# Performance work log

Measured on AMD Instinct MI355X. Metric: run time of the kernel, lower is better.

## Reference

```python
import jax, jax.numpy as jnp
import numpy as np

NUM_HEADS = 8
NUM_GROUPS = 32
EPS = 1e-5

def group_norm(x, w, b):
    B, C, H, W = x.shape
    xg = x.reshape(B, NUM_GROUPS, -1)
    mean = xg.mean(axis=-1, keepdims=True)
    var = xg.var(axis=-1, keepdims=True)
    xg = (xg - mean) * jax.lax.rsqrt(var + EPS)
    return xg.reshape(B, C, H, W) * w[None, :, None, None] + b[None, :, None, None]

def setup_inputs() -> dict:
    key = jax.random.key(0)
    ks = jax.random.split(key, 3)
    B, C, H, W = 16, 512, 32, 32
    x = jax.random.normal(ks[0], (B, C, H, W), dtype=jnp.float32)
    norm_w = jnp.ones((C,), jnp.float32)
    norm_b = jnp.zeros((C,), jnp.float32)
    qkv_w = jax.random.normal(ks[1], (3 * C, C), dtype=jnp.float32) * (C ** -0.5)
    qkv_b = jnp.zeros((3 * C,), jnp.float32)
    proj_w = jax.random.normal(ks[2], (C, C), dtype=jnp.float32) * (C ** -0.5)
    proj_b = jnp.zeros((C,), jnp.float32)
    return {"x": x, "norm_w": norm_w, "norm_b": norm_b, "qkv_w": qkv_w,
            "qkv_b": qkv_b, "proj_w": proj_w, "proj_b": proj_b}

def reference(x, norm_w, norm_b, qkv_w, qkv_b, proj_w, proj_b):
    B, C, H, W = x.shape
    nh, hd = NUM_HEADS, C // NUM_HEADS
    L = H * W
    h = group_norm(x, norm_w, norm_b)
    # 1x1 conv == channel matmul
    qkv = jnp.einsum('oc,bcl->bol', qkv_w, h.reshape(B, C, L)) + qkv_b[None, :, None]
    qkv = qkv.reshape(B, 3, nh, hd, L)
    qkv = jnp.transpose(qkv, (1, 0, 2, 4, 3))  # (3, B, nh, L, hd)
    q, k, v = qkv[0], qkv[1], qkv[2]
    scale = hd ** -0.5
    attn = jax.nn.softmax(jnp.einsum('bnqd,bnkd->bnqk', q, k) * scale, axis=-1)
    h = jnp.einsum('bnqk,bnkd->bnqd', attn, v)          # (B, nh, L, hd)
    h = jnp.transpose(h, (0, 1, 3, 2)).reshape(B, C, L)  # (B, C, L)
    h = jnp.einsum('oc,bcl->bol', proj_w, h) + proj_b[None, :, None]
    return h.reshape(B, C, H, W) + x
```

## Files before the change

kernel.cpp:

```cpp
#include <hip/hip_runtime.h>
#include <hip/hip_bf16.h>

#define BATCH 16
#define CCH   512
#define LSEQ  1024
#define NH    8
#define HD    64
#define NG    32
#define CPG   16
#define EPS   1e-5f

typedef __attribute__((ext_vector_type(8))) short short8;
typedef __attribute__((ext_vector_type(4))) float f32x4;
#define MFMA __builtin_amdgcn_mfma_f32_16x16x32_bf16

__device__ inline short f2bf(float f) {
  unsigned u = __float_as_uint(f);
  u += 0x7FFFu + ((u >> 16) & 1u);
  return (short)(u >> 16);
}

__device__ inline void gl2lds16(const short* g, short* l) {
  __builtin_amdgcn_global_load_lds(
      (const __attribute__((address_space(1))) unsigned*)g,
      (__attribute__((address_space(3))) unsigned*)l, 16, 0, 0);
}
#define VMCNT0() asm volatile("s_waitcnt vmcnt(0)" ::: "memory")

__global__ __launch_bounds__(256) void cvt_kernel(const float* __restrict__ src,
                                                  short* __restrict__ dst) {
  const int i = blockIdx.x * 256 + threadIdx.x;
  const float4 v = ((const float4*)src)[i];
  short vals[4] = {f2bf(v.x), f2bf(v.y), f2bf(v.z), f2bf(v.w)};
  *(uint2*)(dst + (size_t)i * 4) = *(uint2*)vals;
}

__global__ __launch_bounds__(256) void gn_kernel(
    const float* __restrict__ x, const float* __restrict__ nw,
    const float* __restrict__ nb, short* __restrict__ hT)
{
  const int g = blockIdx.x, b = blockIdx.y;
  const size_t base = ((size_t)b * CCH + (size_t)g * CPG) * LSEQ;
  const float4* __restrict__ x4 = (const float4*)(x + base);
  const int tid = threadIdx.x;

  __shared__ short T[16][1026];
  __shared__ float red0[4], red1[4];

  float4 v[16];
  float s = 0.f, s2 = 0.f;
#pragma unroll
  for (int r = 0; r < 16; ++r) {
    v[r] = x4[tid + 256 * r];
    s  += (v[r].x + v[r].y) + (v[r].z + v[r].w);
    s2 += (v[r].x * v[r].x + v[r].y * v[r].y) + (v[r].z * v[r].z + v[r].w * v[r].w);
  }
#pragma unroll
  for (int m = 1; m < 64; m <<= 1) { s += __shfl_xor(s, m); s2 += __shfl_xor(s2, m); }
  const int wid = tid >> 6;
  if ((tid & 63) == 0) { red0[wid] = s; red1[wid] = s2; }
  __syncthreads();
  const float ts  = (red0[0] + red0[1]) + (red0[2] + red0[3]);
  const float ts2 = (red1[0] + red1[1]) + (red1[2] + red1[3]);
  const float mean = ts * (1.f / 16384.f);
  const float var  = ts2 * (1.f / 16384.f) - mean * mean;
  const float rstd = rsqrtf(var + EPS);
#pragma unroll
  for (int r = 0; r < 16; ++r) {
    const int e = tid + 256 * r;
    const int c = e >> 8, l4 = (e & 255) * 4;
    const float sc = rstd * nw[g * CPG + c];
    const float sh = nb[g * CPG + c] - mean * sc;
    T[c][l4 + 0] = f2bf(v[r].x * sc + sh);
    T[c][l4 + 1] = f2bf(v[r].y * sc + sh);
    T[c][l4 + 2] = f2bf(v[r].z * sc + sh);
    T[c][l4 + 3] = f2bf(v[r].w * sc + sh);
  }
  __syncthreads();
  short* __restrict__ outp = hT + (size_t)b * LSEQ * CCH + g * CPG;
#pragma unroll
  for (int it = 0; it < 4; ++it) {
    const int l = tid + 256 * it;
    short vals[16];
#pragma unroll
    for (int c = 0; c < 16; ++c) vals[c] = T[c][l];
    *(short8*)(outp + (size_t)l * CCH)     = *(short8*)&vals[0];
    *(short8*)(outp + (size_t)l * CCH + 8) = *(short8*)&vals[8];
  }
}

__global__ __launch_bounds__(256) void qkv_gemm(
    const short* __restrict__ Wb, const float* __restrict__ bias,
    const short* __restrict__ hT, short* __restrict__ qT,
    short* __restrict__ kT, short* __restrict__ vv)
{
  const int b = blockIdx.z, my = blockIdx.y;
  const int m0 = my * 128, n0 = blockIdx.x * 128;
  const short* __restrict__ Bsrc = hT + (size_t)b * LSEQ * CCH;

  __shared__ short smem[32768];
  const int tid = threadIdx.x, lane = tid & 63, w = tid >> 6;
  const int wm = (w >> 1) * 64, wn = (w & 1) * 64;
  const int l15 = lane & 15, l4g = lane >> 4;
  const int sr = lane >> 3, c8 = ((lane & 7) ^ (lane >> 3)) * 8;
  const int swz = (l15 & 7) << 4;

  const f32x4 fz = {0.f, 0.f, 0.f, 0.f};
  f32x4 acc[4][4];
#pragma unroll
  for (int i = 0; i < 4; ++i)
#pragma unroll
    for (int j = 0; j < 4; ++j) acc[i][j] = fz;

#define QSTAGE(ks, bb)                                                        \
  {                                                                           \
    const int k0_ = (ks) * 64;                                                \
    _Pragma("unroll")                                                         \
    for (int i_ = 0; i_ < 4; ++i_) {                                          \
      const int rb_ = w * 32 + i_ * 8;                                        \
      gl2lds16(Wb   + (size_t)(m0 + rb_ + sr) * CCH + k0_ + c8,               \
               &smem[(bb) * 8192 + rb_ * 64]);                                \
      gl2lds16(Bsrc + (size_t)(n0 + rb_ + sr) * CCH + k0_ + c8,               \
               &smem[16384 + (bb) * 8192 + rb_ * 64]);                        \
    }                                                                         \
  }

  QSTAGE(0, 0);
  VMCNT0();
  __syncthreads();

  for (int ks = 0; ks < 8; ++ks) {
    const int bb = ks & 1;
    if (ks < 7) QSTAGE(ks + 1, bb ^ 1);
#pragma unroll
    for (int kk = 0; kk < 2; ++kk) {
      const int ko = (kk * 64 + l4g * 16) ^ swz;
      short8 af[4], bf[4];
#pragma unroll
      for (int i = 0; i < 4; ++i)
        af[i] = *(const short8*)((const char*)&smem[bb * 8192 + (wm + i * 16 + l15) * 64] + ko);
#pragma unroll
      for (int j = 0; j < 4; ++j)
        bf[j] = *(const short8*)((const char*)&smem[16384 + bb * 8192 + (wn + j * 16 + l15) * 64] + ko);
#pragma unroll
      for (int i = 0; i < 4; ++i)
#pragma unroll
        for (int j = 0; j < 4; ++j)
          acc[i][j] = MFMA(af[i], bf[j], acc[i][j], 0, 0, 0);
    }
    VMCNT0();
    __syncthreads();
  }

  const int region = my >> 2;
  const float scale = (region == 0) ? 0.125f : 1.0f;
  short (*CT)[136] = (short (*)[136])smem;

#pragma unroll
  for (int i = 0; i < 4; ++i)
#pragma unroll
    for (int r = 0; r < 4; ++r) {
      const int cl = wm + i * 16 + l4g * 4 + r;
      const float bb = bias[m0 + cl];
#pragma unroll
      for (int j = 0; j < 4; ++j) {
        const int ll = wn + j * 16 + l15;
        const short bv = f2bf((acc[i][j][r] + bb) * scale);
        if (region == 2) CT[cl][ll] = bv; else CT[ll][cl] = bv;
      }
    }
  __syncthreads();
#pragma unroll
  for (int it = 0; it < 8; ++it) {
    const int f = tid + it * 256;
    const int rr = f >> 4, cc8 = (f & 15) * 8;
    const short8 val = *(const short8*)&CT[rr][cc8];
    if (region == 2) {
      *(short8*)(vv + (size_t)b * CCH * LSEQ + (size_t)((my & 3) * 128 + rr) * LSEQ + n0 + cc8) = val;
    } else {
      short* __restrict__ dst = (region == 0) ? qT : kT;
      *(short8*)(dst + (size_t)b * LSEQ * CCH + (size_t)(n0 + rr) * CCH + (my & 3) * 128 + cc8) = val;
    }
  }
}

__global__ __launch_bounds__(256) void attn_kernel(
    const short* __restrict__ qT, const short* __restrict__ kT,
    const short* __restrict__ vv, short* __restrict__ oT)
{
  const int qt = blockIdx.x, hh = blockIdx.y, b = blockIdx.z;
  const int l0 = qt * 64, h64 = hh * 64;
  const int tid = threadIdx.x, lane = tid & 63, w = tid >> 6;
  const int l15 = lane & 15, l4g = lane >> 4;
  const int wq = w * 16;

  __shared__ short Ks[2][64][64];
  __shared__ short Vs[2][64][64];
  __shared__ unsigned Pw[4][16][36];

  const short* __restrict__ qb = qT + (size_t)b * LSEQ * CCH;
  const short* __restrict__ kb = kT + (size_t)b * LSEQ * CCH;
  const short* __restrict__ vb = vv + (size_t)b * CCH * LSEQ;

  short8 qf[2];
#pragma unroll
  for (int kk = 0; kk < 2; ++kk)
    qf[kk] = *(const short8*)(qb + (size_t)(l0 + wq + l15) * CCH + h64 + kk * 32 + l4g * 8);

  const f32x4 fz = {0.f, 0.f, 0.f, 0.f};
  f32x4 o[4];
#pragma unroll
  for (int df = 0; df < 4; ++df) o[df] = fz;
  float mr = -1.0e30f, lr = 0.f;

  const int sr = lane >> 3, c8 = ((lane & 7) ^ (lane >> 3)) * 8;
  const int swz = (l15 & 7) << 4;

#define ASTAGE(jt_, bb)                                                       \
  {                                                                           \
    const int j0_ = (jt_) * 64;                                               \
    _Pragma("unroll")                                                         \
    for (int i_ = 0; i_ < 2; ++i_) {                                          \
      const int rb_ = w * 16 + i_ * 8;                                        \
      gl2lds16(kb + (size_t)(j0_ + rb_ + sr) * CCH + h64 + c8,                \
               &Ks[bb][rb_][0]);                                              \
      gl2lds16(vb + (size_t)(h64 + rb_ + sr) * LSEQ + j0_ + c8,               \
               &Vs[bb][rb_][0]);                                              \
    }                                                                         \
  }

  ASTAGE(0, 0);
  VMCNT0();
  __syncthreads();

  for (int jt = 0; jt < 16; ++jt) {
    const int bb = jt & 1;
    if (jt < 15) ASTAGE(jt + 1, bb ^ 1);

    f32x4 s[4];
#pragma unroll
    for (int j = 0; j < 4; ++j) s[j] = fz;
#pragma unroll
    for (int kk = 0; kk < 2; ++kk) {
      const int ko = (kk * 64 + l4g * 16) ^ swz;
      short8 kf[4];
#pragma unroll
      for (int j = 0; j < 4; ++j)
        kf[j] = *(const short8*)((const char*)&Ks[bb][j * 16 + l15][0] + ko);
#pragma unroll
      for (int j = 0; j < 4; ++j) s[j] = MFMA(kf[j], qf[kk], s[j], 0, 0, 0);
    }

    float mx = s[0][0];
#pragma unroll
    for (int j = 0; j < 4; ++j)
#pragma unroll
      for (int r = 0; r < 4; ++r) mx = fmaxf(mx, s[j][r]);
    mx = fmaxf(mx, __shfl_xor(mx, 16));
    mx = fmaxf(mx, __shfl_xor(mx, 32));
    const float mnew = fmaxf(mr, mx);
    const float corr = __expf(mr - mnew);
    mr = mnew;

    float rs = 0.f;
    unsigned pk[4][2];
#pragma unroll
    for (int j = 0; j < 4; ++j) {
      float p0 = __expf(s[j][0] - mnew), p1 = __expf(s[j][1] - mnew);
      float p2 = __expf(s[j][2] - mnew), p3 = __expf(s[j][3] - mnew);
      rs += (p0 + p1) + (p2 + p3);
      __hip_bfloat162 w0 = __float22bfloat162_rn(make_float2(p0, p1));
      __hip_bfloat162 w1 = __float22bfloat162_rn(make_float2(p2, p3));
      pk[j][0] = *(unsigned*)&w0;
      pk[j][1] = *(unsigned*)&w1;
    }
    rs += __shfl_xor(rs, 16);
    rs += __shfl_xor(rs, 32);
    lr = lr * corr + rs;

#pragma unroll
    for (int j = 0; j < 4; ++j)
      *(uint2*)&Pw[w][l15][j * 8 + l4g * 2] = make_uint2(pk[j][0], pk[j][1]);

    float cb[4];
#pragma unroll
    for (int r = 0; r < 4; ++r) cb[r] = __shfl(corr, l4g * 4 + r);
#pragma unroll
    for (int df = 0; df < 4; ++df)
#pragma unroll
      for (int r = 0; r < 4; ++r) o[df][r] *= cb[r];

#pragma unroll
    for (int kk = 0; kk < 2; ++kk) {
      const short8 pf = *(const short8*)&Pw[w][l15][kk * 16 + l4g * 4];
      const int ko = (kk * 64 + l4g * 16) ^ swz;
#pragma unroll
      for (int df = 0; df < 4; ++df) {
        const short8 vf = *(const short8*)((const char*)&Vs[bb][df * 16 + l15][0] + ko);
        o[df] = MFMA(pf, vf, o[df], 0, 0, 0);
      }
    }
    VMCNT0();
    __syncthreads();
  }

  float lb[4];
#pragma unroll
  for (int r = 0; r < 4; ++r) lb[r] = 1.f / __shfl(lr, l4g * 4 + r);
  short* __restrict__ ob = oT + (size_t)b * LSEQ * CCH;
#pragma unroll
  for (int df = 0; df < 4; ++df)
#pragma unroll
    for (int r = 0; r < 4; ++r)
      ob[(size_t)(l0 + wq + l4g * 4 + r) * CCH + h64 + df * 16 + l15] = f2bf(o[df][r] * lb[r]);
}

__global__ __launch_bounds__(256) void proj_gemm(
    const short* __restrict__ Wb, const float* __restrict__ bias,
    const short* __restrict__ oT, const float* __restrict__ x,
    float* __restrict__ out)
{
  const int b = blockIdx.z;
  const int m0 = blockIdx.y * 128, n0 = blockIdx.x * 128;
  const short* __restrict__ Bsrc = oT + (size_t)b * LSEQ * CCH;

  __shared__ short smem[32768];
  const int tid = threadIdx.x, lane = tid & 63, w = tid >> 6;
  const int wm = (w >> 1) * 64, wn = (w & 1) * 64;
  const int l15 = lane & 15, l4g = lane >> 4;
  const int sr = lane >> 3, c8 = ((lane & 7) ^ (lane >> 3)) * 8;
  const int swz = (l15 & 7) << 4;

  const f32x4 fz = {0.f, 0.f, 0.f, 0.f};
  f32x4 acc[4][4];
#pragma unroll
  for (int i = 0; i < 4; ++i)
#pragma unroll
    for (int j = 0; j < 4; ++j) acc[i][j] = fz;

#define PSTAGE(ks, bb)                                                        \
  {                                                                           \
    const int k0_ = (ks) * 64;                                                \
    _Pragma("unroll")                                                         \
    for (int i_ = 0; i_ < 4; ++i_) {                                          \
      const int rb_ = w * 32 + i_ * 8;                                        \
      gl2lds16(Wb   + (size_t)(m0 + rb_ + sr) * CCH + k0_ + c8,               \
               &smem[(bb) * 8192 + rb_ * 64]);                                \
      gl2lds16(Bsrc + (size_t)(n0 + rb_ + sr) * CCH + k0_ + c8,               \
               &smem[16384 + (bb) * 8192 + rb_ * 64]);                        \
    }                                                                         \
  }

  PSTAGE(0, 0);
  VMCNT0();
  __syncthreads();

  for (int ks = 0; ks < 8; ++ks) {
    const int bb = ks & 1;
    if (ks < 7) PSTAGE(ks + 1, bb ^ 1);
#pragma unroll
    for (int kk = 0; kk < 2; ++kk) {
      const int ko = (kk * 64 + l4g * 16) ^ swz;
      short8 af[4], bf[4];
#pragma unroll
      for (int i = 0; i < 4; ++i)
        af[i] = *(const short8*)((const char*)&smem[bb * 8192 + (wm + i * 16 + l15) * 64] + ko);
#pragma unroll
      for (int j = 0; j < 4; ++j)
        bf[j] = *(const short8*)((const char*)&smem[16384 + bb * 8192 + (wn + j * 16 + l15) * 64] + ko);
#pragma unroll
      for (int i = 0; i < 4; ++i)
#pragma unroll
        for (int j = 0; j < 4; ++j)
          acc[i][j] = MFMA(af[i], bf[j], acc[i][j], 0, 0, 0);
    }
    VMCNT0();
    __syncthreads();
  }

  const size_t obase = (size_t)b * CCH * LSEQ;
#pragma unroll
  for (int i = 0; i < 4; ++i)
#pragma unroll
    for (int r = 0; r < 4; ++r) {
      const int gm = m0 + wm + i * 16 + l4g * 4 + r;
      const float bb = bias[gm];
#pragma unroll
      for (int j = 0; j < 4; ++j) {
        const int gl = n0 + wn + j * 16 + l15;
        const size_t idx = obase + (size_t)gm * LSEQ + gl;
        out[idx] = acc[i][j][r] + bb + x[idx];
      }
    }
}

extern "C" void kernel_launch(void* const* d_in, const int* in_sizes, int n_in,
                              void* d_out, int out_size, void* d_ws, size_t ws_size,
                              hipStream_t stream)
{
  const float* x      = (const float*)d_in[0];
  const float* norm_w = (const float*)d_in[1];
  const float* norm_b = (const float*)d_in[2];
  const float* qkv_w  = (const float*)d_in[3];
  const float* qkv_b  = (const float*)d_in[4];
  const float* proj_w = (const float*)d_in[5];
  const float* proj_b = (const float*)d_in[6];
  float* out = (float*)d_out;

  char* ws = (char*)d_ws;
  short* wq16 = (short*)ws;
  short* wp16 = (short*)(ws + 1572864);
  short* hT   = (short*)(ws + 2097152);
  short* qT   = (short*)(ws + 2097152 + 16777216);
  short* kT   = (short*)(ws + 2097152 + 2 * 16777216);
  short* vv   = (short*)(ws + 2097152 + 3 * 16777216);
  short* oT   = (short*)(ws + 2097152 + 4 * 16777216);

  cvt_kernel<<<768, 256, 0, stream>>>(qkv_w, wq16);
  cvt_kernel<<<256, 256, 0, stream>>>(proj_w, wp16);
  gn_kernel<<<dim3(NG, BATCH), 256, 0, stream>>>(x, norm_w, norm_b, hT);
  qkv_gemm<<<dim3(8, 12, BATCH), 256, 0, stream>>>(wq16, qkv_b, hT, qT, kT, vv);
  attn_kernel<<<dim3(16, NH, BATCH), 256, 0, stream>>>(qT, kT, vv, oT);
  proj_gemm<<<dim3(8, 4, BATCH), 256, 0, stream>>>(wp16, proj_b, oT, x, out);
}
```

Before: 243.1 us.

## Rewrite attention with 32x32 MFMA, 128-query tiles and register-resident P

The attention kernel now uses 32x32x16 bf16 MFMA with each wave owning 32 query rows, so a block covers 128 queries and K/V tiles loaded into LDS are reused across twice as many queries. The P matrix is no longer round-tripped through LDS: it is rearranged between lane halves with cross-lane shuffles and fed straight to the PV MFMA. Softmax switches to exp2 with log2(e) folded into the Q scale in the QKV GEMM epilogue, and the row max and sum reductions happen mostly in-register. The grid is flattened so blocks sharing a (batch, head) are adjacent. The cost is higher register pressure from 16-wide accumulators and half as many blocks, which may lower occupancy.

```diff
diff --git a/kernel.cpp b/kernel.cpp
--- a/kernel.cpp
+++ b/kernel.cpp
@@ -12,7 +12,9 @@
 
 typedef __attribute__((ext_vector_type(8))) short short8;
 typedef __attribute__((ext_vector_type(4))) float f32x4;
-#define MFMA __builtin_amdgcn_mfma_f32_16x16x32_bf16
+typedef __attribute__((ext_vector_type(16))) float f32x16;
+#define MFMA   __builtin_amdgcn_mfma_f32_16x16x32_bf16
+#define MFMA32 __builtin_amdgcn_mfma_f32_32x32x16_bf16
 
 __device__ inline short f2bf(float f) {
   unsigned u = __float_as_uint(f);
@@ -153,7 +155,7 @@
   }
 
   const int region = my >> 2;
-  const float scale = (region == 0) ? 0.125f : 1.0f;
+  const float scale = (region == 0) ? 0.125f * 1.44269504f : 1.0f;
   short (*CT)[136] = (short (*)[136])smem;
 
 #pragma unroll
@@ -188,33 +190,31 @@
     const short* __restrict__ qT, const short* __restrict__ kT,
     const short* __restrict__ vv, short* __restrict__ oT)
 {
-  const int qt = blockIdx.x, hh = blockIdx.y, b = blockIdx.z;
-  const int l0 = qt * 64, h64 = hh * 64;
+  const int id = blockIdx.x;
+  const int qt = id >> 7, bhh = id & 127;
+  const int hh = bhh & 7, b = bhh >> 3;
+  const int l0 = qt * 128, h64 = hh * 64;
   const int tid = threadIdx.x, lane = tid & 63, w = tid >> 6;
-  const int l15 = lane & 15, l4g = lane >> 4;
-  const int wq = w * 16;
+  const int l31 = lane & 31, hi = lane >> 5;
+  const int wq = w * 32;
 
   __shared__ short Ks[2][64][64];
   __shared__ short Vs[2][64][64];
-  __shared__ unsigned Pw[4][16][36];
 
   const short* __restrict__ qb = qT + (size_t)b * LSEQ * CCH;
   const short* __restrict__ kb = kT + (size_t)b * LSEQ * CCH;
   const short* __restrict__ vb = vv + (size_t)b * CCH * LSEQ;
 
-  short8 qf[2];
-#pragma unroll
-  for (int kk = 0; kk < 2; ++kk)
-    qf[kk] = *(const short8*)(qb + (size_t)(l0 + wq + l15) * CCH + h64 + kk * 32 + l4g * 8);
-
-  const f32x4 fz = {0.f, 0.f, 0.f, 0.f};
-  f32x4 o[4];
-#pragma unroll
-  for (int df = 0; df < 4; ++df) o[df] = fz;
+  short8 qf[4];
+#pragma unroll
+  for (int t = 0; t < 4; ++t)
+    qf[t] = *(const short8*)(qb + (size_t)(l0 + wq + l31) * CCH + h64 + t * 16 + hi * 8);
+
+  f32x16 oacc0 = {0.f,0.f,0.f,0.f,0.f,0.f,0.f,0.f,0.f,0.f,0.f,0.f,0.f,0.f,0.f,0.f};
+  f32x16 oacc1 = oacc0;
   float mr = -1.0e30f, lr = 0.f;
 
   const int sr = lane >> 3, c8 = ((lane & 7) ^ (lane >> 3)) * 8;
-  const int swz = (l15 & 7) << 4;
 
 #define ASTAGE(jt_, bb)                                                       \
   {                                                                           \
@@ -237,82 +237,99 @@
     const int bb = jt & 1;
     if (jt < 15) ASTAGE(jt + 1, bb ^ 1);
 
-    f32x4 s[4];
-#pragma unroll
-    for (int j = 0; j < 4; ++j) s[j] = fz;
-#pragma unroll
-    for (int kk = 0; kk < 2; ++kk) {
-      const int ko = (kk * 64 + l4g * 16) ^ swz;
-      short8 kf[4];
-#pragma unroll
-      for (int j = 0; j < 4; ++j)
-        kf[j] = *(const short8*)((const char*)&Ks[bb][j * 16 + l15][0] + ko);
-#pragma unroll
-      for (int j = 0; j < 4; ++j) s[j] = MFMA(kf[j], qf[kk], s[j], 0, 0, 0);
-    }
-
-    float mx = s[0][0];
-#pragma unroll
-    for (int j = 0; j < 4; ++j)
-#pragma unroll
-      for (int r = 0; r < 4; ++r) mx = fmaxf(mx, s[j][r]);
-    mx = fmaxf(mx, __shfl_xor(mx, 16));
+    f32x16 s0 = {0.f,0.f,0.f,0.f,0.f,0.f,0.f,0.f,0.f,0.f,0.f,0.f,0.f,0.f,0.f,0.f};
+    f32x16 s1 = s0;
+#pragma unroll
+    for (int t = 0; t < 4; ++t) {
+      const int byt = ((t * 2 + hi) ^ (l31 & 7)) * 16;
+      const short8 k0 = *(const short8*)((const char*)&Ks[bb][l31][0] + byt);
+      const short8 k1 = *(const short8*)((const char*)&Ks[bb][32 + l31][0] + byt);
+      s0 = MFMA32(k0, qf[t], s0, 0, 0, 0);
+      s1 = MFMA32(k1, qf[t], s1, 0, 0, 0);
+    }
+
+    float t16[16];
+#pragma unroll
+    for (int i = 0; i < 16; ++i) t16[i] = fmaxf(s0[i], s1[i]);
+#pragma unroll
+    for (int st = 8; st > 0; st >>= 1)
+#pragma unroll
+      for (int i = 0; i < 8; ++i)
+        if (i < st) t16[i] = fmaxf(t16[i], t16[i + st]);
+    float mx = t16[0];
     mx = fmaxf(mx, __shfl_xor(mx, 32));
     const float mnew = fmaxf(mr, mx);
-    const float corr = __expf(mr - mnew);
+    const float corr = exp2f(mr - mnew);
     mr = mnew;
 
-    float rs = 0.f;
-    unsigned pk[4][2];
-#pragma unroll
-    for (int j = 0; j < 4; ++j) {
-      float p0 = __expf(s[j][0] - mnew), p1 = __expf(s[j][1] - mnew);
-      float p2 = __expf(s[j][2] - mnew), p3 = __expf(s[j][3] - mnew);
-      rs += (p0 + p1) + (p2 + p3);
-      __hip_bfloat162 w0 = __float22bfloat162_rn(make_float2(p0, p1));
-      __hip_bfloat162 w1 = __float22bfloat162_rn(make_float2(p2, p3));
-      pk[j][0] = *(unsigned*)&w0;
-      pk[j][1] = *(unsigned*)&w1;
-    }
-    rs += __shfl_xor(rs, 16);
+#pragma unroll
+    for (int i = 0; i < 16; ++i) {
+      s0[i] = exp2f(s0[i] - mnew);
+      s1[i] = exp2f(s1[i] - mnew);
+    }
+    float a16[16];
+#pragma unroll
+    for (int i = 0; i < 16; ++i) a16[i] = s0[i] + s1[i];
+#pragma unroll
+    for (int st = 8; st > 0; st >>= 1)
+#pragma unroll
+      for (int i = 0; i < 8; ++i)
+        if (i < st) a16[i] += a16[i + st];
+    float rs = a16[0];
     rs += __shfl_xor(rs, 32);
     lr = lr * corr + rs;
 
-#pragma unroll
-    for (int j = 0; j < 4; ++j)
-      *(uint2*)&Pw[w][l15][j * 8 + l4g * 2] = make_uint2(pk[j][0], pk[j][1]);
-
-    float cb[4];
-#pragma unroll
-    for (int r = 0; r < 4; ++r) cb[r] = __shfl(corr, l4g * 4 + r);
-#pragma unroll
-    for (int df = 0; df < 4; ++df)
-#pragma unroll
-      for (int r = 0; r < 4; ++r) o[df][r] *= cb[r];
-
-#pragma unroll
-    for (int kk = 0; kk < 2; ++kk) {
-      const short8 pf = *(const short8*)&Pw[w][l15][kk * 16 + l4g * 4];
-      const int ko = (kk * 64 + l4g * 16) ^ swz;
-#pragma unroll
-      for (int df = 0; df < 4; ++df) {
-        const short8 vf = *(const short8*)((const char*)&Vs[bb][df * 16 + l15][0] + ko);
-        o[df] = MFMA(pf, vf, o[df], 0, 0, 0);
-      }
+    unsigned wpk[16];
+#pragma unroll
+    for (int j = 0; j < 8; ++j) {
+      __hip_bfloat162 pa = __float22bfloat162_rn(make_float2(s0[2 * j], s0[2 * j + 1]));
+      __hip_bfloat162 pb = __float22bfloat162_rn(make_float2(s1[2 * j], s1[2 * j + 1]));
+      wpk[j]     = *(unsigned*)&pa;
+      wpk[8 + j] = *(unsigned*)&pb;
+    }
+
+#pragma unroll
+    for (int i = 0; i < 16; ++i) { oacc0[i] *= corr; oacc1[i] *= corr; }
+
+#pragma unroll
+    for (int kt = 0; kt < 4; ++kt) {
+      const int jb = (kt >> 1) * 8 + (kt & 1) * 4;
+      const unsigned vs0 = hi ? wpk[jb + 0] : wpk[jb + 2];
+      const unsigned vs1 = hi ? wpk[jb + 1] : wpk[jb + 3];
+      const unsigned r0 = (unsigned)__shfl_xor((int)vs0, 32);
+      const unsigned r1 = (unsigned)__shfl_xor((int)vs1, 32);
+      union { unsigned u[4]; short8 s; } pf;
+      pf.u[0] = hi ? r0 : wpk[jb + 0];
+      pf.u[1] = hi ? r1 : wpk[jb + 1];
+      pf.u[2] = hi ? wpk[jb + 2] : r0;
+      pf.u[3] = hi ? wpk[jb + 3] : r1;
+      const int byt = ((kt * 2 + hi) ^ (l31 & 7)) * 16;
+      const short8 v0 = *(const short8*)((const char*)&Vs[bb][l31][0] + byt);
+      const short8 v1 = *(const short8*)((const char*)&Vs[bb][32 + l31][0] + byt);
+      oacc0 = MFMA32(v0, pf.s, oacc0, 0, 0, 0);
+      oacc1 = MFMA32(v1, pf.s, oacc1, 0, 0, 0);
     }
     VMCNT0();
     __syncthreads();
   }
 
-  float lb[4];
-#pragma unroll
-  for (int r = 0; r < 4; ++r) lb[r] = 1.f / __shfl(lr, l4g * 4 + r);
-  short* __restrict__ ob = oT + (size_t)b * LSEQ * CCH;
-#pragma unroll
-  for (int df = 0; df < 4; ++df)
-#pragma unroll
-    for (int r = 0; r < 4; ++r)
-      ob[(size_t)(l0 + wq + l4g * 4 + r) * CCH + h64 + df * 16 + l15] = f2bf(o[df][r] * lb[r]);
+  const float lb = 1.f / lr;
+  short* __restrict__ ob = oT + (size_t)b * LSEQ * CCH + (size_t)(l0 + wq + l31) * CCH + h64;
+#pragma unroll
+  for (int rg = 0; rg < 4; ++rg) {
+    __hip_bfloat162 w0 = __float22bfloat162_rn(
+        make_float2(oacc0[rg * 4 + 0] * lb, oacc0[rg * 4 + 1] * lb));
+    __hip_bfloat162 w1 = __float22bfloat162_rn(
+        make_float2(oacc0[rg * 4 + 2] * lb, oacc0[rg * 4 + 3] * lb));
+    uint2 pk0 = make_uint2(*(unsigned*)&w0, *(unsigned*)&w1);
+    *(uint2*)(ob + rg * 8 + hi * 4) = pk0;
+    __hip_bfloat162 w2 = __float22bfloat162_rn(
+        make_float2(oacc1[rg * 4 + 0] * lb, oacc1[rg * 4 + 1] * lb));
+    __hip_bfloat162 w3 = __float22bfloat162_rn(
+        make_float2(oacc1[rg * 4 + 2] * lb, oacc1[rg * 4 + 3] * lb));
+    uint2 pk1 = make_uint2(*(unsigned*)&w2, *(unsigned*)&w3);
+    *(uint2*)(ob + 32 + rg * 8 + hi * 4) = pk1;
+  }
 }
 
 __global__ __launch_bounds__(256) void proj_gemm(
@@ -420,6 +437,6 @@
   cvt_kernel<<<256, 256, 0, stream>>>(proj_w, wp16);
   gn_kernel<<<dim3(NG, BATCH), 256, 0, stream>>>(x, norm_w, norm_b, hT);
   qkv_gemm<<<dim3(8, 12, BATCH), 256, 0, stream>>>(wq16, qkv_b, hT, qT, kT, vv);
-  attn_kernel<<<dim3(16, NH, BATCH), 256, 0, stream>>>(qT, kT, vv, oT);
+  attn_kernel<<<1024, 256, 0, stream>>>(qT, kT, vv, oT);
   proj_gemm<<<dim3(8, 4, BATCH), 256, 0, stream>>>(wp16, proj_b, oT, x, out);
 }
```

New measurement: 289.8 us. 1.19x slower.
